# Optimization experiments

Hardware: AMD Instinct MI355X
Metric: run time of the kernel (lower is better)

The kernel has to match this reference:

```python
import jax, jax.numpy as jnp
import numpy as np

N, C, K, H = 131072, 512, 128, 8  # points, channels, patch_size, heads


def setup_inputs() -> dict:
    key = jax.random.key(0)
    ks = jax.random.split(key, 6)
    feat = jax.random.normal(ks[0], (N, C), dtype=jnp.float32)
    Wqkv = jax.random.normal(ks[1], (C, 3 * C), dtype=jnp.float32) * 0.02
    bqkv = jax.random.normal(ks[2], (3 * C,), dtype=jnp.float32) * 0.02
    Wproj = jax.random.normal(ks[3], (C, C), dtype=jnp.float32) * 0.02
    bproj = jax.random.normal(ks[4], (C,), dtype=jnp.float32) * 0.02
    order = jax.random.permutation(ks[5], N).astype(jnp.int64)  # serialized order (all clusters full)
    inverse = jnp.argsort(order).astype(jnp.int64)              # serialized inverse
    return {"feat": feat, "Wqkv": Wqkv, "bqkv": bqkv, "Wproj": Wproj,
            "bproj": bproj, "order": order, "inverse": inverse}


def reference(feat, Wqkv, bqkv, Wproj, bproj, order, inverse):
    hd = C // H
    scale = hd ** -0.5
    qkv = feat @ Wqkv + bqkv                 # [N, 3C]
    qkv = qkv[order]                         # gather by serialized order
    qkv = qkv.reshape(-1, K, 3, H, hd)       # [W, K, 3, H, hd]
    qkv = jnp.moveaxis(qkv, 2, 0)            # [3, W, K, H, hd]
    q = jnp.swapaxes(qkv[0], 1, 2)           # [W, H, K, hd]
    k = jnp.swapaxes(qkv[1], 1, 2)
    v = jnp.swapaxes(qkv[2], 1, 2)
    # upcast_attention / upcast_softmax -> compute scores & softmax in fp32
    attn = jnp.einsum('whkd,whjd->whkj', (q * scale).astype(jnp.float32),
                      k.astype(jnp.float32))             # [W, H, K, K]
    attn = jax.nn.softmax(attn, axis=-1).astype(feat.dtype)
    out = jnp.einsum('whkj,whjd->whkd', attn, v)          # [W, H, K, hd]
    out = jnp.swapaxes(out, 1, 2).reshape(-1, C)          # [N, C]
    out = out[inverse]                                    # scatter back via inverse
    out = out @ Wproj + bproj
    return out
```

## Files before the change

### kernel.cpp

```cpp
#include <hip/hip_runtime.h>
#include <hip/hip_bf16.h>
#include <cstdint>
#include <cstddef>

typedef __bf16 bf16;
typedef __bf16 bf16x8 __attribute__((ext_vector_type(8)));
typedef float f32x4 __attribute__((ext_vector_type(4)));

#define N_PTS 131072
#define CDIM  512
#define C3    1536
#define HD    64
#define NH    8
#define KWIN  128

static __device__ __forceinline__ bf16 cvt(float x) { return (bf16)x; }

static __device__ __forceinline__ void gld16(const bf16* g, bf16* l) {
    __builtin_amdgcn_global_load_lds(
        (const __attribute__((address_space(1))) void*)g,
        (__attribute__((address_space(3))) void*)l, 16, 0, 0);
}

__global__ __launch_bounds__(256) void k_prep(
    const float* __restrict__ Wqkv, const float* __restrict__ Wproj,
    bf16* __restrict__ Wqkv_t, bf16* __restrict__ Wproj_t)
{
    int idx = blockIdx.x * 256 + threadIdx.x;
    if (idx < CDIM * C3) {
        int k = idx / C3, c = idx % C3;
        Wqkv_t[(size_t)c * CDIM + k] = cvt(Wqkv[idx]);
    } else {
        int j = idx - CDIM * C3;
        if (j < CDIM * CDIM) {
            int k = j / CDIM, c = j % CDIM;
            Wproj_t[(size_t)c * CDIM + k] = cvt(Wproj[j]);
        }
    }
}

__global__ __launch_bounds__(256) void k_gather(
    const float* __restrict__ feat, const int* __restrict__ order,
    bf16* __restrict__ feat_g)
{
    int row = blockIdx.x * 2 + (threadIdx.x >> 7);
    int c   = (threadIdx.x & 127) << 2;
    int src = order[row];
    float4 v = *reinterpret_cast<const float4*>(feat + (size_t)src * CDIM + c);
    union { bf16 e[4]; uint2 u; } pk;
    pk.e[0] = cvt(v.x); pk.e[1] = cvt(v.y); pk.e[2] = cvt(v.z); pk.e[3] = cvt(v.w);
    *reinterpret_cast<uint2*>(feat_g + (size_t)row * CDIM + c) = pk.u;
}

template <bool F32OUT, int NT>
__global__ __launch_bounds__(512) void k_gemm(
    const bf16* __restrict__ Ag, const bf16* __restrict__ Bt,
    const float* __restrict__ bias, void* __restrict__ outp)
{
    __shared__ __align__(16) bf16 As[4][256 * 32];
    __shared__ __align__(16) bf16 Bs[4][256 * 32];

    const int t    = threadIdx.x;
    const int lane = t & 63;
    const int wv   = t >> 6;
    const int wr   = wv >> 2;
    const int wc   = wv & 3;
    const int g    = lane >> 4, r16 = lane & 15;

    const int nwg = gridDim.x;
    const int bid = blockIdx.x;
    const int swz = (bid & 7) * (nwg >> 3) + (bid >> 3);
    const int m0  = (swz / NT) * 256;
    const int n0  = (swz % NT) * 256;

    const int L0 = wv * 64 + lane;
    const int L1 = L0 + 512;
    const bf16* sA0 = Ag + (size_t)(m0 + (L0 >> 2)) * CDIM + (L0 & 3) * 8;
    const bf16* sA1 = Ag + (size_t)(m0 + (L1 >> 2)) * CDIM + (L1 & 3) * 8;
    const bf16* sB0 = Bt + (size_t)(n0 + (L0 >> 2)) * CDIM + (L0 & 3) * 8;
    const bf16* sB1 = Bt + (size_t)(n0 + (L1 >> 2)) * CDIM + (L1 & 3) * 8;

    int aoff[8], boff[4];
#pragma unroll
    for (int i = 0; i < 8; ++i) {
        int row = wr * 128 + i * 16 + r16;
        aoff[i] = row * 64 + g * 16;
    }
#pragma unroll
    for (int n = 0; n < 4; ++n) {
        int row = wc * 64 + n * 16 + r16;
        boff[n] = row * 64 + g * 16;
    }

    f32x4 acc[8][4];
    const f32x4 z = {0.f, 0.f, 0.f, 0.f};
#pragma unroll
    for (int i = 0; i < 8; ++i)
#pragma unroll
        for (int n = 0; n < 4; ++n) acc[i][n] = z;

    auto stage = [&](int kt) {
        const int b  = kt & 3;
        const int ko = kt * 32;
        gld16(sA0 + ko, &As[b][(size_t)wv * 64 * 8]);
        gld16(sA1 + ko, &As[b][(size_t)(512 + wv * 64) * 8]);
        gld16(sB0 + ko, &Bs[b][(size_t)wv * 64 * 8]);
        gld16(sB1 + ko, &Bs[b][(size_t)(512 + wv * 64) * 8]);
    };

    auto compute = [&](int kt) {
        const int b = kt & 3;
        bf16x8 af[8], bv[4];
#pragma unroll
        for (int i = 0; i < 8; ++i)
            af[i] = *reinterpret_cast<const bf16x8*>(
                reinterpret_cast<const char*>(&As[b][0]) + aoff[i]);
#pragma unroll
        for (int n = 0; n < 4; ++n)
            bv[n] = *reinterpret_cast<const bf16x8*>(
                reinterpret_cast<const char*>(&Bs[b][0]) + boff[n]);
        asm volatile("s_waitcnt lgkmcnt(0)" ::: "memory");
        __builtin_amdgcn_sched_barrier(0);
        __builtin_amdgcn_s_setprio(1);
#pragma unroll
        for (int i = 0; i < 8; ++i)
#pragma unroll
            for (int n = 0; n < 4; ++n)
                acc[i][n] = __builtin_amdgcn_mfma_f32_16x16x32_bf16(
                    af[i], bv[n], acc[i][n], 0, 0, 0);
        __builtin_amdgcn_s_setprio(0);
    };

    stage(0); stage(1); stage(2);
    asm volatile("s_waitcnt vmcnt(8)" ::: "memory");
    __builtin_amdgcn_s_barrier();
    __builtin_amdgcn_sched_barrier(0);

#pragma unroll
    for (int kt = 0; kt < 13; ++kt) {
        stage(kt + 3);
        compute(kt);
        asm volatile("s_waitcnt vmcnt(8)" ::: "memory");
        __builtin_amdgcn_s_barrier();
        __builtin_amdgcn_sched_barrier(0);
    }
    compute(13);
    asm volatile("s_waitcnt vmcnt(4)" ::: "memory");
    __builtin_amdgcn_s_barrier();
    __builtin_amdgcn_sched_barrier(0);
    compute(14);
    asm volatile("s_waitcnt vmcnt(0)" ::: "memory");
    __builtin_amdgcn_s_barrier();
    __builtin_amdgcn_sched_barrier(0);
    compute(15);

    const int ldo = NT * 256;
#pragma unroll
    for (int n = 0; n < 4; ++n) {
        int col = n0 + wc * 64 + n * 16 + r16;
        float b = bias[col];
#pragma unroll
        for (int i = 0; i < 8; ++i)
#pragma unroll
            for (int j = 0; j < 4; ++j) {
                int row = m0 + wr * 128 + i * 16 + g * 4 + j;
                if (F32OUT)
                    reinterpret_cast<float*>(outp)[(size_t)row * ldo + col] =
                        acc[i][n][j] + b;
                else
                    reinterpret_cast<bf16*>(outp)[(size_t)row * ldo + col] =
                        cvt(acc[i][n][j] + b);
            }
    }
}

__global__ __launch_bounds__(256) void k_attn(
    const bf16* __restrict__ qkv_s, const int* __restrict__ order,
    bf16* __restrict__ attn_g)
{
    __shared__ __align__(16) char smem[36864 + 64 * 136 * 2];
    __shared__ int ord_s[KWIN];
    bf16 (*Q)[72]   = reinterpret_cast<bf16 (*)[72]>(smem);
    bf16 (*Kt)[72]  = reinterpret_cast<bf16 (*)[72]>(smem + 128 * 72 * 2);
    bf16 (*P)[136]  = reinterpret_cast<bf16 (*)[136]>(smem);
    bf16 (*Vt)[136] = reinterpret_cast<bf16 (*)[136]>(smem + 36864);

    const int t    = threadIdx.x;
    const int lane = t & 63;
    const int wv   = t >> 6;
    const int g    = lane >> 4, r16 = lane & 15;
    const int h    = blockIdx.x;
    const int w    = blockIdx.y;

    const bf16* base = qkv_s + (size_t)w * KWIN * C3 + h * HD;

    if (t < KWIN) ord_s[t] = order[w * KWIN + t];

#pragma unroll
    for (int it = 0; it < 4; ++it) {
        int s   = it * 256 + t;
        int tok = s >> 3;
        int c8  = (s & 7) << 3;
        size_t roff = (size_t)tok * C3 + c8;
        *reinterpret_cast<uint4*>(&Q[tok][c8])  =
            *reinterpret_cast<const uint4*>(base + roff);
        *reinterpret_cast<uint4*>(&Kt[tok][c8]) =
            *reinterpret_cast<const uint4*>(base + roff + CDIM);
        uint4 vvec = *reinterpret_cast<const uint4*>(base + roff + 2 * CDIM);
        const bf16* ve = reinterpret_cast<const bf16*>(&vvec);
#pragma unroll
        for (int i = 0; i < 8; ++i) Vt[c8 + i][tok] = ve[i];
    }
    __syncthreads();

    f32x4 sc[2][8];
    const f32x4 z = {0.f, 0.f, 0.f, 0.f};
#pragma unroll
    for (int m = 0; m < 2; ++m)
#pragma unroll
        for (int n = 0; n < 8; ++n) sc[m][n] = z;

#pragma unroll
    for (int ks = 0; ks < 2; ++ks) {
        bf16x8 aq[2];
#pragma unroll
        for (int m = 0; m < 2; ++m)
            aq[m] = *reinterpret_cast<const bf16x8*>(
                &Q[wv * 32 + m * 16 + r16][ks * 32 + g * 8]);
#pragma unroll
        for (int n = 0; n < 8; ++n) {
            bf16x8 bk = *reinterpret_cast<const bf16x8*>(
                &Kt[n * 16 + r16][ks * 32 + g * 8]);
#pragma unroll
            for (int m = 0; m < 2; ++m)
                sc[m][n] = __builtin_amdgcn_mfma_f32_16x16x32_bf16(
                    aq[m], bk, sc[m][n], 0, 0, 0);
        }
    }

    const float scale = 0.125f;
    float inv_sum[2][4];
#pragma unroll
    for (int m = 0; m < 2; ++m) {
#pragma unroll
        for (int j = 0; j < 4; ++j) {
            float mx = -3.0e38f;
#pragma unroll
            for (int n = 0; n < 8; ++n) mx = fmaxf(mx, sc[m][n][j]);
            mx = fmaxf(mx, __shfl_xor(mx, 1));
            mx = fmaxf(mx, __shfl_xor(mx, 2));
            mx = fmaxf(mx, __shfl_xor(mx, 4));
            mx = fmaxf(mx, __shfl_xor(mx, 8));
            mx *= scale;
            float ssum = 0.f;
#pragma unroll
            for (int n = 0; n < 8; ++n) {
                float p = __expf(sc[m][n][j] * scale - mx);
                sc[m][n][j] = p;
                ssum += p;
            }
            ssum += __shfl_xor(ssum, 1);
            ssum += __shfl_xor(ssum, 2);
            ssum += __shfl_xor(ssum, 4);
            ssum += __shfl_xor(ssum, 8);
            inv_sum[m][j] = 1.f / ssum;
        }
    }

    __syncthreads();

#pragma unroll
    for (int m = 0; m < 2; ++m)
#pragma unroll
        for (int n = 0; n < 8; ++n)
#pragma unroll
            for (int j = 0; j < 4; ++j)
                P[wv * 32 + m * 16 + g * 4 + j][n * 16 + r16] =
                    cvt(sc[m][n][j] * inv_sum[m][j]);

    f32x4 o[2][4];
#pragma unroll
    for (int m = 0; m < 2; ++m)
#pragma unroll
        for (int n = 0; n < 4; ++n) o[m][n] = z;

#pragma unroll
    for (int kt = 0; kt < 4; ++kt) {
        bf16x8 ap[2];
#pragma unroll
        for (int m = 0; m < 2; ++m)
            ap[m] = *reinterpret_cast<const bf16x8*>(
                &P[wv * 32 + m * 16 + r16][kt * 32 + g * 8]);
#pragma unroll
        for (int n = 0; n < 4; ++n) {
            bf16x8 bv = *reinterpret_cast<const bf16x8*>(
                &Vt[n * 16 + r16][kt * 32 + g * 8]);
#pragma unroll
            for (int m = 0; m < 2; ++m)
                o[m][n] = __builtin_amdgcn_mfma_f32_16x16x32_bf16(
                    ap[m], bv, o[m][n], 0, 0, 0);
        }
    }

#pragma unroll
    for (int m = 0; m < 2; ++m)
#pragma unroll
        for (int n = 0; n < 4; ++n)
#pragma unroll
            for (int j = 0; j < 4; ++j) {
                int tok  = wv * 32 + m * 16 + g * 4 + j;
                int d    = n * 16 + r16;
                int drow = ord_s[tok];
                attn_g[(size_t)drow * CDIM + h * HD + d] = cvt(o[m][n][j]);
            }
}

extern "C" void kernel_launch(void* const* d_in, const int* in_sizes, int n_in,
                              void* d_out, int out_size, void* d_ws, size_t ws_size,
                              hipStream_t stream)
{
    const float* feat    = (const float*)d_in[0];
    const float* Wqkv    = (const float*)d_in[1];
    const float* bqkv    = (const float*)d_in[2];
    const float* Wproj   = (const float*)d_in[3];
    const float* bproj   = (const float*)d_in[4];
    const int*   order   = (const int*)d_in[5];
    float* out = (float*)d_out;

    const size_t qkv_bytes  = (size_t)N_PTS * C3 * sizeof(bf16);
    const size_t gat_bytes  = (size_t)N_PTS * CDIM * sizeof(bf16);
    const size_t wq_bytes   = (size_t)C3 * CDIM * sizeof(bf16);
    const size_t wp_bytes   = (size_t)CDIM * CDIM * sizeof(bf16);
    if (ws_size < qkv_bytes + gat_bytes + wq_bytes + wp_bytes) return;

    bf16* qkv_s     = (bf16*)d_ws;
    bf16* shared134 = (bf16*)((char*)d_ws + qkv_bytes);
    bf16* Wqkv_t    = (bf16*)((char*)d_ws + qkv_bytes + gat_bytes);
    bf16* Wproj_t   = (bf16*)((char*)d_ws + qkv_bytes + gat_bytes + wq_bytes);

    k_prep<<<dim3((CDIM * C3 + CDIM * CDIM + 255) / 256), 256, 0, stream>>>(
        Wqkv, Wproj, Wqkv_t, Wproj_t);
    k_gather<<<dim3(N_PTS / 2), 256, 0, stream>>>(feat, order, shared134);
    k_gemm<false, C3 / 256><<<dim3((N_PTS / 256) * (C3 / 256)), 512, 0, stream>>>(
        shared134, Wqkv_t, bqkv, qkv_s);
    k_attn<<<dim3(NH, N_PTS / KWIN), 256, 0, stream>>>(qkv_s, order, shared134);
    k_gemm<true, CDIM / 256><<<dim3((N_PTS / 256) * (CDIM / 256)), 512, 0, stream>>>(
        shared134, Wproj_t, bproj, out);
}
```

Before: 664.8 us.

## Swizzle GEMM LDS tiles and use a 3-stage split A/B pipeline

The GEMM's LDS ring buffer shrinks from 4 stages to 3, and the A and B tile loads are issued separately, each interleaved with half of the MFMA work per k-step. LDS chunks are XOR-style rotated by row on both the global-to-LDS copy and the fragment reads, to reduce bank conflicts on the ds_read path. launch_bounds(512,2) is added to try for two workgroups per CU. The risks are that the register cap may force spills of the 128-float accumulator, and LDS use may still be too large for two workgroups per CU.

```diff
diff --git a/kernel.cpp b/kernel.cpp
--- a/kernel.cpp
+++ b/kernel.cpp
@@ -53,12 +53,12 @@
 }
 
 template <bool F32OUT, int NT>
-__global__ __launch_bounds__(512) void k_gemm(
+__global__ __launch_bounds__(512, 2) void k_gemm(
     const bf16* __restrict__ Ag, const bf16* __restrict__ Bt,
     const float* __restrict__ bias, void* __restrict__ outp)
 {
-    __shared__ __align__(16) bf16 As[4][256 * 32];
-    __shared__ __align__(16) bf16 Bs[4][256 * 32];
+    __shared__ __align__(16) bf16 As[3][256 * 32];
+    __shared__ __align__(16) bf16 Bs[3][256 * 32];
 
     const int t    = threadIdx.x;
     const int lane = t & 63;
@@ -74,22 +74,23 @@
     const int n0  = (swz % NT) * 256;
 
     const int L0 = wv * 64 + lane;
-    const int L1 = L0 + 512;
-    const bf16* sA0 = Ag + (size_t)(m0 + (L0 >> 2)) * CDIM + (L0 & 3) * 8;
-    const bf16* sA1 = Ag + (size_t)(m0 + (L1 >> 2)) * CDIM + (L1 & 3) * 8;
-    const bf16* sB0 = Bt + (size_t)(n0 + (L0 >> 2)) * CDIM + (L0 & 3) * 8;
-    const bf16* sB1 = Bt + (size_t)(n0 + (L1 >> 2)) * CDIM + (L1 & 3) * 8;
+    const int r0 = L0 >> 2,        s0 = ((L0 & 3) - (r0 >> 1)) & 3;
+    const int r1 = r0 + 128,       s1 = ((L0 & 3) - (r1 >> 1)) & 3;
+    const bf16* srcA0 = Ag + (size_t)(m0 + r0) * CDIM + s0 * 8;
+    const bf16* srcA1 = Ag + (size_t)(m0 + r1) * CDIM + s1 * 8;
+    const bf16* srcB0 = Bt + (size_t)(n0 + r0) * CDIM + s0 * 8;
+    const bf16* srcB1 = Bt + (size_t)(n0 + r1) * CDIM + s1 * 8;
 
     int aoff[8], boff[4];
 #pragma unroll
     for (int i = 0; i < 8; ++i) {
         int row = wr * 128 + i * 16 + r16;
-        aoff[i] = row * 64 + g * 16;
+        aoff[i] = row * 64 + (((g + (row >> 1)) & 3) << 4);
     }
 #pragma unroll
     for (int n = 0; n < 4; ++n) {
         int row = wc * 64 + n * 16 + r16;
-        boff[n] = row * 64 + g * 16;
+        boff[n] = row * 64 + (((g + (row >> 1)) & 3) << 4);
     }
 
     f32x4 acc[8][4];
@@ -99,60 +100,77 @@
 #pragma unroll
         for (int n = 0; n < 4; ++n) acc[i][n] = z;
 
-    auto stage = [&](int kt) {
-        const int b  = kt & 3;
-        const int ko = kt * 32;
-        gld16(sA0 + ko, &As[b][(size_t)wv * 64 * 8]);
-        gld16(sA1 + ko, &As[b][(size_t)(512 + wv * 64) * 8]);
-        gld16(sB0 + ko, &Bs[b][(size_t)wv * 64 * 8]);
-        gld16(sB1 + ko, &Bs[b][(size_t)(512 + wv * 64) * 8]);
+    const int NKT = CDIM / 32;
+
+    auto stageA = [&](int s) {
+        const int b  = s % 3;
+        const int ko = s * 32;
+        gld16(srcA0 + ko, &As[b][(size_t)wv * 64 * 8]);
+        gld16(srcA1 + ko, &As[b][(size_t)(512 + wv * 64) * 8]);
     };
-
-    auto compute = [&](int kt) {
-        const int b = kt & 3;
-        bf16x8 af[8], bv[4];
-#pragma unroll
-        for (int i = 0; i < 8; ++i)
-            af[i] = *reinterpret_cast<const bf16x8*>(
-                reinterpret_cast<const char*>(&As[b][0]) + aoff[i]);
+    auto stageB = [&](int s) {
+        const int b  = s % 3;
+        const int ko = s * 32;
+        gld16(srcB0 + ko, &Bs[b][(size_t)wv * 64 * 8]);
+        gld16(srcB1 + ko, &Bs[b][(size_t)(512 + wv * 64) * 8]);
+    };
+
+    stageA(0); stageB(0); stageA(1); stageB(1);
+    asm volatile("s_waitcnt vmcnt(4)" ::: "memory");
+    __builtin_amdgcn_s_barrier();
+    __builtin_amdgcn_sched_barrier(0);
+
+#pragma unroll
+    for (int s = 0; s < NKT; ++s) {
+        const int b = s % 3;
+        const char* abase = reinterpret_cast<const char*>(&As[b][0]);
+        const char* bbase = reinterpret_cast<const char*>(&Bs[b][0]);
+
+        bf16x8 af0[4], bv[4];
+#pragma unroll
+        for (int i = 0; i < 4; ++i)
+            af0[i] = *reinterpret_cast<const bf16x8*>(abase + aoff[i]);
 #pragma unroll
         for (int n = 0; n < 4; ++n)
-            bv[n] = *reinterpret_cast<const bf16x8*>(
-                reinterpret_cast<const char*>(&Bs[b][0]) + boff[n]);
+            bv[n] = *reinterpret_cast<const bf16x8*>(bbase + boff[n]);
+        if (s < NKT - 2) stageA(s + 2);
+        __builtin_amdgcn_s_barrier();
         asm volatile("s_waitcnt lgkmcnt(0)" ::: "memory");
         __builtin_amdgcn_sched_barrier(0);
         __builtin_amdgcn_s_setprio(1);
 #pragma unroll
-        for (int i = 0; i < 8; ++i)
+        for (int i = 0; i < 4; ++i)
 #pragma unroll
             for (int n = 0; n < 4; ++n)
                 acc[i][n] = __builtin_amdgcn_mfma_f32_16x16x32_bf16(
-                    af[i], bv[n], acc[i][n], 0, 0, 0);
+                    af0[i], bv[n], acc[i][n], 0, 0, 0);
         __builtin_amdgcn_s_setprio(0);
-    };
-
-    stage(0); stage(1); stage(2);
-    asm volatile("s_waitcnt vmcnt(8)" ::: "memory");
-    __builtin_amdgcn_s_barrier();
-    __builtin_amdgcn_sched_barrier(0);
-
-#pragma unroll
-    for (int kt = 0; kt < 13; ++kt) {
-        stage(kt + 3);
-        compute(kt);
-        asm volatile("s_waitcnt vmcnt(8)" ::: "memory");
         __builtin_amdgcn_s_barrier();
         __builtin_amdgcn_sched_barrier(0);
-    }
-    compute(13);
-    asm volatile("s_waitcnt vmcnt(4)" ::: "memory");
-    __builtin_amdgcn_s_barrier();
-    __builtin_amdgcn_sched_barrier(0);
-    compute(14);
-    asm volatile("s_waitcnt vmcnt(0)" ::: "memory");
-    __builtin_amdgcn_s_barrier();
-    __builtin_amdgcn_sched_barrier(0);
-    compute(15);
+
+        bf16x8 af1[4];
+#pragma unroll
+        for (int i = 0; i < 4; ++i)
+            af1[i] = *reinterpret_cast<const bf16x8*>(abase + aoff[4 + i]);
+        if (s < NKT - 2) stageB(s + 2);
+        __builtin_amdgcn_s_barrier();
+        asm volatile("s_waitcnt lgkmcnt(0)" ::: "memory");
+        __builtin_amdgcn_sched_barrier(0);
+        __builtin_amdgcn_s_setprio(1);
+#pragma unroll
+        for (int i = 0; i < 4; ++i)
+#pragma unroll
+            for (int n = 0; n < 4; ++n)
+                acc[4 + i][n] = __builtin_amdgcn_mfma_f32_16x16x32_bf16(
+                    af1[i], bv[n], acc[4 + i][n], 0, 0, 0);
+        __builtin_amdgcn_s_setprio(0);
+        if (s < NKT - 2)
+            asm volatile("s_waitcnt vmcnt(4)" ::: "memory");
+        else if (s == NKT - 2)
+            asm volatile("s_waitcnt vmcnt(0)" ::: "memory");
+        __builtin_amdgcn_s_barrier();
+        __builtin_amdgcn_sched_barrier(0);
+    }
 
     const int ldo = NT * 256;
 #pragma unroll
```

Measured after the change: 640.7 us. 1.04x faster.

## Restructure GEMM mainloop with BK=64 double buffering, swizzled LDS and register prefetch

Applied to the files above, without the earlier changes.

Restructures the GEMM main loop to use 64-wide K tiles with two LDS buffers instead of four 32-wide buffers. Rows in LDS are XOR-swizzled to avoid bank conflicts. The inner loop is split into four phases that prefetch the next A/B fragments into registers while MFMAs run, and the global loads for tile tau+2 are issued mid-iteration. The aim is to hide LDS read latency and cut barriers per K element, at the cost of more registers and a more intricate wait and barrier schedule.

```diff
diff --git a/kernel.cpp b/kernel.cpp
--- a/kernel.cpp
+++ b/kernel.cpp
@@ -53,12 +53,12 @@
 }
 
 template <bool F32OUT, int NT>
-__global__ __launch_bounds__(512) void k_gemm(
+__global__ __launch_bounds__(512) void k_gemm8(
     const bf16* __restrict__ Ag, const bf16* __restrict__ Bt,
     const float* __restrict__ bias, void* __restrict__ outp)
 {
-    __shared__ __align__(16) bf16 As[4][256 * 32];
-    __shared__ __align__(16) bf16 Bs[4][256 * 32];
+    __shared__ __align__(16) bf16 As[2][256 * 64];
+    __shared__ __align__(16) bf16 Bs[2][256 * 64];
 
     const int t    = threadIdx.x;
     const int lane = t & 63;
@@ -73,24 +73,43 @@
     const int m0  = (swz / NT) * 256;
     const int n0  = (swz % NT) * 256;
 
-    const int L0 = wv * 64 + lane;
-    const int L1 = L0 + 512;
-    const bf16* sA0 = Ag + (size_t)(m0 + (L0 >> 2)) * CDIM + (L0 & 3) * 8;
-    const bf16* sA1 = Ag + (size_t)(m0 + (L1 >> 2)) * CDIM + (L1 & 3) * 8;
-    const bf16* sB0 = Bt + (size_t)(n0 + (L0 >> 2)) * CDIM + (L0 & 3) * 8;
-    const bf16* sB1 = Bt + (size_t)(n0 + (L1 >> 2)) * CDIM + (L1 & 3) * 8;
-
-    int aoff[8], boff[4];
-#pragma unroll
-    for (int i = 0; i < 8; ++i) {
-        int row = wr * 128 + i * 16 + r16;
-        aoff[i] = row * 64 + g * 16;
-    }
-#pragma unroll
-    for (int n = 0; n < 4; ++n) {
-        int row = wc * 64 + n * 16 + r16;
-        boff[n] = row * 64 + g * 16;
-    }
+    const int NKT = CDIM / 64;
+
+    int aSrc[2][2], bSrc[2][2];
+    int dstE[2][2];
+#pragma unroll
+    for (int h = 0; h < 2; ++h)
+#pragma unroll
+        for (int j = 0; j < 2; ++j) {
+            int L = wv * 128 + j * 64 + lane;
+            int row_l = L >> 3, p8 = L & 7;
+            int s8 = (p8 - (row_l & 7)) & 7;
+            int grow = h * 128 + row_l;
+            aSrc[h][j] = (m0 + grow) * CDIM + s8 * 8;
+            bSrc[h][j] = (n0 + grow) * CDIM + s8 * 8;
+            dstE[h][j] = h * 8192 + (wv * 128 + j * 64) * 8;
+        }
+
+    int aoff[2][2][4];
+    int boff[2][4];
+#pragma unroll
+    for (int grp = 0; grp < 2; ++grp)
+#pragma unroll
+        for (int kh = 0; kh < 2; ++kh)
+#pragma unroll
+            for (int q = 0; q < 4; ++q) {
+                int row = wr * 128 + (grp * 4 + q) * 16 + r16;
+                aoff[grp][kh][q] = row * 128 +
+                    (((kh * 4 + g + (r16 & 7)) & 7) << 4);
+            }
+#pragma unroll
+    for (int kh = 0; kh < 2; ++kh)
+#pragma unroll
+        for (int n = 0; n < 4; ++n) {
+            int row = wc * 64 + n * 16 + r16;
+            boff[kh][n] = row * 128 +
+                (((kh * 4 + g + (r16 & 7)) & 7) << 4);
+        }
 
     f32x4 acc[8][4];
     const f32x4 z = {0.f, 0.f, 0.f, 0.f};
@@ -99,60 +118,83 @@
 #pragma unroll
         for (int n = 0; n < 4; ++n) acc[i][n] = z;
 
-    auto stage = [&](int kt) {
-        const int b  = kt & 3;
-        const int ko = kt * 32;
-        gld16(sA0 + ko, &As[b][(size_t)wv * 64 * 8]);
-        gld16(sA1 + ko, &As[b][(size_t)(512 + wv * 64) * 8]);
-        gld16(sB0 + ko, &Bs[b][(size_t)wv * 64 * 8]);
-        gld16(sB1 + ko, &Bs[b][(size_t)(512 + wv * 64) * 8]);
+    bf16x8 afr[2][4], bfr[2][4];
+
+    auto stageA = [&](int tau) {
+        const int b = tau & 1, ko = tau * 64;
+#pragma unroll
+        for (int h = 0; h < 2; ++h)
+#pragma unroll
+            for (int j = 0; j < 2; ++j)
+                gld16(Ag + aSrc[h][j] + ko, &As[b][dstE[h][j]]);
     };
-
-    auto compute = [&](int kt) {
-        const int b = kt & 3;
-        bf16x8 af[8], bv[4];
-#pragma unroll
-        for (int i = 0; i < 8; ++i)
-            af[i] = *reinterpret_cast<const bf16x8*>(
-                reinterpret_cast<const char*>(&As[b][0]) + aoff[i]);
+    auto stageB = [&](int tau) {
+        const int b = tau & 1, ko = tau * 64;
+#pragma unroll
+        for (int h = 0; h < 2; ++h)
+#pragma unroll
+            for (int j = 0; j < 2; ++j)
+                gld16(Bt + bSrc[h][j] + ko, &Bs[b][dstE[h][j]]);
+    };
+    auto readA = [&](int set, int b, int grp, int kh) {
+        const char* ab = reinterpret_cast<const char*>(&As[b][0]);
+#pragma unroll
+        for (int q = 0; q < 4; ++q)
+            afr[set][q] = *reinterpret_cast<const bf16x8*>(ab + aoff[grp][kh][q]);
+    };
+    auto readB = [&](int b, int kh) {
+        const char* bb = reinterpret_cast<const char*>(&Bs[b][0]);
 #pragma unroll
         for (int n = 0; n < 4; ++n)
-            bv[n] = *reinterpret_cast<const bf16x8*>(
-                reinterpret_cast<const char*>(&Bs[b][0]) + boff[n]);
-        asm volatile("s_waitcnt lgkmcnt(0)" ::: "memory");
-        __builtin_amdgcn_sched_barrier(0);
-        __builtin_amdgcn_s_setprio(1);
-#pragma unroll
-        for (int i = 0; i < 8; ++i)
-#pragma unroll
-            for (int n = 0; n < 4; ++n)
-                acc[i][n] = __builtin_amdgcn_mfma_f32_16x16x32_bf16(
-                    af[i], bv[n], acc[i][n], 0, 0, 0);
-        __builtin_amdgcn_s_setprio(0);
+            bfr[kh][n] = *reinterpret_cast<const bf16x8*>(bb + boff[kh][n]);
     };
 
-    stage(0); stage(1); stage(2);
+    stageB(0); stageA(0); stageB(1); stageA(1);
     asm volatile("s_waitcnt vmcnt(8)" ::: "memory");
     __builtin_amdgcn_s_barrier();
+    readA(0, 0, 0, 0);
+    readB(0, 0);
+    asm volatile("s_waitcnt lgkmcnt(0)" ::: "memory");
     __builtin_amdgcn_sched_barrier(0);
 
 #pragma unroll
-    for (int kt = 0; kt < 13; ++kt) {
-        stage(kt + 3);
-        compute(kt);
-        asm volatile("s_waitcnt vmcnt(8)" ::: "memory");
-        __builtin_amdgcn_s_barrier();
-        __builtin_amdgcn_sched_barrier(0);
-    }
-    compute(13);
-    asm volatile("s_waitcnt vmcnt(4)" ::: "memory");
-    __builtin_amdgcn_s_barrier();
-    __builtin_amdgcn_sched_barrier(0);
-    compute(14);
-    asm volatile("s_waitcnt vmcnt(0)" ::: "memory");
-    __builtin_amdgcn_s_barrier();
-    __builtin_amdgcn_sched_barrier(0);
-    compute(15);
+    for (int tau = 0; tau < NKT; ++tau) {
+#pragma unroll
+        for (int p = 0; p < 4; ++p) {
+            const int pi  = tau * 4 + p;
+            const int grp = p & 1, kh = p >> 1;
+
+            if (p == 2 && tau + 2 < NKT) stageB(tau + 2);
+            if (p == 3 && tau + 2 < NKT) stageA(tau + 2);
+
+            if (pi + 1 < NKT * 4) {
+                const int pn   = (p + 1) & 3;
+                const int taun = tau + (p == 3);
+                const int bn   = taun & 1;
+                readA((pi + 1) & 1, bn, pn & 1, pn >> 1);
+                if (pn == 0 || pn == 2) readB(bn, pn >> 1);
+            }
+
+            __builtin_amdgcn_s_setprio(1);
+#pragma unroll
+            for (int q = 0; q < 4; ++q)
+#pragma unroll
+                for (int n = 0; n < 4; ++n)
+                    acc[grp * 4 + q][n] = __builtin_amdgcn_mfma_f32_16x16x32_bf16(
+                        afr[pi & 1][q], bfr[kh][n], acc[grp * 4 + q][n], 0, 0, 0);
+            __builtin_amdgcn_s_setprio(0);
+
+            asm volatile("s_waitcnt lgkmcnt(0)" ::: "memory");
+            __builtin_amdgcn_sched_barrier(0);
+            if (p == 2) {
+                if (tau + 2 < NKT)
+                    asm volatile("s_waitcnt vmcnt(4)" ::: "memory");
+                else
+                    asm volatile("s_waitcnt vmcnt(0)" ::: "memory");
+            }
+            __builtin_amdgcn_s_barrier();
+        }
+    }
 
     const int ldo = NT * 256;
 #pragma unroll
@@ -293,12 +335,12 @@
                 &P[wv * 32 + m * 16 + r16][kt * 32 + g * 8]);
 #pragma unroll
         for (int n = 0; n < 4; ++n) {
-            bf16x8 bv = *reinterpret_cast<const bf16x8*>(
+            bf16x8 bvv = *reinterpret_cast<const bf16x8*>(
                 &Vt[n * 16 + r16][kt * 32 + g * 8]);
 #pragma unroll
             for (int m = 0; m < 2; ++m)
                 o[m][n] = __builtin_amdgcn_mfma_f32_16x16x32_bf16(
-                    ap[m], bv, o[m][n], 0, 0, 0);
+                    ap[m], bvv, o[m][n], 0, 0, 0);
         }
     }
 
@@ -327,10 +369,10 @@
     const int*   order   = (const int*)d_in[5];
     float* out = (float*)d_out;
 
-    const size_t qkv_bytes  = (size_t)N_PTS * C3 * sizeof(bf16);
-    const size_t gat_bytes  = (size_t)N_PTS * CDIM * sizeof(bf16);
-    const size_t wq_bytes   = (size_t)C3 * CDIM * sizeof(bf16);
-    const size_t wp_bytes   = (size_t)CDIM * CDIM * sizeof(bf16);
+    const size_t qkv_bytes = (size_t)N_PTS * C3 * sizeof(bf16);
+    const size_t gat_bytes = (size_t)N_PTS * CDIM * sizeof(bf16);
+    const size_t wq_bytes  = (size_t)C3 * CDIM * sizeof(bf16);
+    const size_t wp_bytes  = (size_t)CDIM * CDIM * sizeof(bf16);
     if (ws_size < qkv_bytes + gat_bytes + wq_bytes + wp_bytes) return;
 
     bf16* qkv_s     = (bf16*)d_ws;
@@ -341,9 +383,9 @@
     k_prep<<<dim3((CDIM * C3 + CDIM * CDIM + 255) / 256), 256, 0, stream>>>(
         Wqkv, Wproj, Wqkv_t, Wproj_t);
     k_gather<<<dim3(N_PTS / 2), 256, 0, stream>>>(feat, order, shared134);
-    k_gemm<false, C3 / 256><<<dim3((N_PTS / 256) * (C3 / 256)), 512, 0, stream>>>(
+    k_gemm8<false, C3 / 256><<<dim3((N_PTS / 256) * (C3 / 256)), 512, 0, stream>>>(
         shared134, Wqkv_t, bqkv, qkv_s);
     k_attn<<<dim3(NH, N_PTS / KWIN), 256, 0, stream>>>(qkv_s, order, shared134);
-    k_gemm<true, CDIM / 256><<<dim3((N_PTS / 256) * (CDIM / 256)), 512, 0, stream>>>(
+    k_gemm8<true, CDIM / 256><<<dim3((N_PTS / 256) * (CDIM / 256)), 512, 0, stream>>>(
         shared134, Wproj_t, bproj, out);
 }
```

Measured after the change: 626.9 us. 5.7% less time.
